# Kernel tuning notes

Hardware: AMD Instinct MI355X
Metric: run time of the kernel (lower is better)

Reference implementation:

```python
import jax, jax.numpy as jnp
import numpy as np

DN = ('NCHW', 'OIHW', 'NCHW')

def conv2d(x, w, b, pad):
    y = jax.lax.conv_general_dilated(x, w, (1, 1), [(pad, pad), (pad, pad)], dimension_numbers=DN)
    return y + b[None, :, None, None]

def setup_inputs() -> dict:
    key = jax.random.key(0)
    ks = jax.random.split(key, 12)
    nc, hc = 10, 16
    B, H, W = 8, 256, 256
    s = 0.1  # small init scale
    return {
        'x': jax.random.normal(ks[0], (B, nc, H, W), dtype=jnp.float32),
        'perceive_w': jax.random.normal(ks[1], (hc * 2, nc + hc, 3, 3), dtype=jnp.float32) * s,
        'perceive_b': jax.random.normal(ks[2], (hc * 2,), dtype=jnp.float32) * s,
        'update1_w': jax.random.normal(ks[3], (hc, hc * 2, 1, 1), dtype=jnp.float32) * s,
        'update1_b': jax.random.normal(ks[4], (hc,), dtype=jnp.float32) * s,
        'update2_w': jax.random.normal(ks[5], (hc, hc, 1, 1), dtype=jnp.float32) * s,
        'update2_b': jax.random.normal(ks[6], (hc,), dtype=jnp.float32) * s,
        'tau_w': jax.random.normal(ks[7], (hc, nc + hc * 2, 3, 3), dtype=jnp.float32) * s,
        'tau_b': jax.random.normal(ks[8], (hc,), dtype=jnp.float32) * s,
        'b_tau': jnp.ones((1, hc, 1, 1), dtype=jnp.float32) * 1.5,
        'readout_w': jax.random.normal(ks[9], (nc, hc, 1, 1), dtype=jnp.float32) * s,
        'readout_b': jax.random.normal(ks[10], (nc,), dtype=jnp.float32) * s,
        'n_steps': 10,
    }

def reference(x, perceive_w, perceive_b, update1_w, update1_b, update2_w, update2_b,
              tau_w, tau_b, b_tau, readout_w, readout_b, n_steps):
    B, _, H, W = x.shape
    hc = update2_w.shape[0]
    state0 = jnp.zeros((B, hc, H, W), dtype=x.dtype)

    def step(state, _):
        combined = jnp.concatenate([x, state], axis=1)          # [B, nc+hc, H, W]
        perception = conv2d(combined, perceive_w, perceive_b, 1)  # [B, 2*hc, H, W]
        hidden = jax.nn.relu(conv2d(perception, update1_w, update1_b, 0))
        delta = conv2d(hidden, update2_w, update2_b, 0)          # [B, hc, H, W]
        tau_input = jnp.concatenate([x, state, delta], axis=1)   # [B, nc+2*hc, H, W]
        beta = jax.nn.sigmoid(conv2d(tau_input, tau_w, tau_b, 1) + b_tau)
        beta = jnp.clip(beta, 0.01, 0.99)
        state = beta * state + (1.0 - beta) * delta
        return state, None

    state, _ = jax.lax.scan(step, state0, None, length=n_steps)
    return conv2d(state, readout_w, readout_b, 0)                # [B, nc, H, W]
```

## Files before the change

### kernel.cpp

```cpp
#include <hip/hip_runtime.h>
#include <math.h>

#define BATCH 8
#define NC 10
#define HC 16
#define HH 256
#define WW 256
#define NSTEPS 10
#define PLANE (HH*WW)

typedef _Float16 v8h  __attribute__((ext_vector_type(8)));
typedef _Float16 v4h  __attribute__((ext_vector_type(4)));
typedef float    v16f __attribute__((ext_vector_type(16)));

#define TW 32
#define TH 8
#define IPW 36
#define IPH 12
#define IPOS (IPW*IPH)
#define ICH 40
#define DPW 34
#define DPH 10
#define DPOS (DPW*DPH)
#define DCH 24

#define MFMA32(A,B,C) __builtin_amdgcn_mfma_f32_32x32x16_f16(A, B, C, 0, 0, 0)

__global__ __launch_bounds__(256) void k_prep(
    const float* __restrict__ x, _Float16* __restrict__ xh)
{
    int g = blockIdx.x * 256 + threadIdx.x;
    int b = g >> 16, pix = g & 65535;
    v8h lo = {0,0,0,0,0,0,0,0}, hi = {0,0,0,0,0,0,0,0};
    #pragma unroll
    for (int c = 0; c < 8; ++c) lo[c] = (_Float16)x[(b*NC + c)*PLANE + pix];
    hi[0] = (_Float16)x[(b*NC + 8)*PLANE + pix];
    hi[1] = (_Float16)x[(b*NC + 9)*PLANE + pix];
    v8h* dst = (v8h*)&xh[(size_t)g * 16];
    dst[0] = lo; dst[1] = hi;
}

__global__ __launch_bounds__(256) void k_repack(
    const float* __restrict__ pw,
    const float* __restrict__ tw,
    const float* __restrict__ u1w, const float* __restrict__ u1b,
    const float* __restrict__ pb,
    const float* __restrict__ u2w,
    _Float16* __restrict__ apD,
    _Float16* __restrict__ apT,
    _Float16* __restrict__ apU1,
    _Float16* __restrict__ apU2,
    float* __restrict__ u1bp)
{
    const int tid = threadIdx.x;
    for (int i = tid; i < 9*2*512; i += 256) {
        int j = i & 7, lane = (i >> 3) & 63, kc = (i >> 9) & 1, t = i >> 10;
        int m = lane & 31, ke = (lane >> 5)*8 + j;
        float v = 0.f;
        if (kc == 1)      v = pw[(m*26 + 10 + ke)*9 + t];
        else if (ke < 10) v = pw[(m*26 + ke)*9 + t];
        apD[i] = (_Float16)v;
    }
    for (int i = tid; i < 9*3*512; i += 256) {
        int j = i & 7, lane = (i >> 3) & 63, r = i >> 9;
        int kc = r % 3, t = r / 3;
        int m = lane & 31, ke = (lane >> 5)*8 + j;
        float v = 0.f;
        if (m < 16) {
            if (kc == 0)      { if (ke < 10) v = tw[(m*42 + ke)*9 + t]; }
            else if (kc == 1) v = tw[(m*42 + 10 + ke)*9 + t];
            else              v = tw[(m*42 + 26 + ke)*9 + t];
        }
        apT[i] = (_Float16)v;
    }
    for (int i = tid; i < 2*2*512; i += 256) {
        int j = i & 7, lane = (i >> 3) & 63, part = (i >> 9) & 1, c = (i >> 10) & 1;
        int m = lane & 31, hh = lane >> 5;
        int ch = 16*c + 4*hh + (j & 3) + 8*(j >> 2);
        float w = (m < 16) ? u1w[m*32 + ch] : 0.f;
        _Float16 hi = (_Float16)w;
        apU1[i] = part ? (_Float16)(w - (float)hi) : hi;
    }
    for (int i = tid; i < 2*512; i += 256) {
        int j = i & 7, lane = (i >> 3) & 63, part = i >> 9;
        int m = lane & 31, hh = lane >> 5;
        int ch = 4*hh + (j & 3) + 8*(j >> 2);
        float w = (m < 16) ? u2w[m*16 + ch] : 0.f;
        _Float16 hi = (_Float16)w;
        apU2[i] = part ? (_Float16)(w - (float)hi) : hi;
    }
    if (tid < 16) {
        float s = u1b[tid];
        for (int p = 0; p < 32; ++p) s += u1w[tid*32 + p] * pb[p];
        u1bp[tid] = s;
    }
}

__device__ __forceinline__ void chain_mfma(
    const v16f A, int p, int h, int by, int bx,
    v8h u1h0, v8h u1r0, v8h u1h1, v8h u1r1,
    v8h u2h, v8h u2r,
    const float* bu1, const float* bu2,
    _Float16* __restrict__ smDl)
{
    v8h b0h, b0r, b1h, b1r;
    #pragma unroll
    for (int j = 0; j < 8; ++j) {
        _Float16 h0 = (_Float16)A[j];
        b0h[j] = h0; b0r[j] = (_Float16)(A[j] - (float)h0);
        _Float16 h1 = (_Float16)A[8 + j];
        b1h[j] = h1; b1r[j] = (_Float16)(A[8 + j] - (float)h1);
    }
    v16f hacc = {0,0,0,0,0,0,0,0,0,0,0,0,0,0,0,0};
    hacc = MFMA32(u1h0, b0h, hacc);
    hacc = MFMA32(u1h0, b0r, hacc);
    hacc = MFMA32(u1r0, b0h, hacc);
    hacc = MFMA32(u1h1, b1h, hacc);
    hacc = MFMA32(u1h1, b1r, hacc);
    hacc = MFMA32(u1r1, b1h, hacc);
    v8h ch_, cr_;
    #pragma unroll
    for (int j = 0; j < 8; ++j) {
        float v = fmaxf(hacc[j] + bu1[j], 0.f);
        _Float16 hh = (_Float16)v;
        ch_[j] = hh; cr_[j] = (_Float16)(v - (float)hh);
    }
    v16f dacc = {0,0,0,0,0,0,0,0,0,0,0,0,0,0,0,0};
    dacc = MFMA32(u2h, ch_, dacc);
    dacc = MFMA32(u2h, cr_, dacc);
    dacc = MFMA32(u2r, ch_, dacc);

    const int yy = p / DPW, xx = p - yy * DPW;
    const int gy = by + yy - 1, gx = bx + xx - 1;
    const bool inImg = (gy >= 0 && gy < HH && gx >= 0 && gx < WW);

    v4h hi0, hi1;
    #pragma unroll
    for (int j = 0; j < 4; ++j) {
        float d0 = inImg ? (dacc[j]     + bu2[j])     : 0.f;
        float d1 = inImg ? (dacc[4 + j] + bu2[4 + j]) : 0.f;
        hi0[j] = (_Float16)d0;
        hi1[j] = (_Float16)d1;
    }
    _Float16* dst = &smDl[p * DCH];
    *(v4h*)(dst + 4*h)     = hi0;
    *(v4h*)(dst + 8 + 4*h) = hi1;
}

__global__ __launch_bounds__(256, 3) void k_step(
    const _Float16* __restrict__ xh,
    const _Float16* __restrict__ shO,
    const _Float16* __restrict__ apD,
    const _Float16* __restrict__ apT,
    const _Float16* __restrict__ apU1,
    const _Float16* __restrict__ apU2,
    const float* __restrict__ u1bp, const float* __restrict__ u2b,
    const float* __restrict__ tb,  const float* __restrict__ btau,
    _Float16* __restrict__ shN,
    const float* __restrict__ rw,  const float* __restrict__ rb,
    float* __restrict__ out, int last)
{
    __shared__ __align__(16) _Float16 smIn[IPOS * ICH];
    __shared__ __align__(16) _Float16 smDl[DPOS * DCH];

    const int tid = threadIdx.x;
    const int bx = blockIdx.x * TW, by = blockIdx.y * TH, b = blockIdx.z;

    for (int i = tid; i < IPOS; i += 256) {
        int yy = i / IPW, xx = i - yy * IPW;
        int gy = by + yy - 2, gx = bx + xx - 2;
        v8h x0 = {0,0,0,0,0,0,0,0}, x1 = x0, s0 = x0, s1 = x0;
        if (gy >= 0 && gy < HH && gx >= 0 && gx < WW) {
            size_t base = ((size_t)((b*HH + gy)*WW + gx)) * 16;
            const v8h* px_ = (const v8h*)&xh[base];
            x0 = px_[0]; x1 = px_[1];
            const v8h* ps_ = (const v8h*)&shO[base];
            s0 = ps_[0]; s1 = ps_[1];
        }
        _Float16* d = &smIn[i * ICH];
        *(v8h*)(d)      = x0;  *(v8h*)(d + 8)  = x1;
        *(v8h*)(d + 16) = s0;  *(v8h*)(d + 24) = s1;
    }

    const int lane = tid & 63, w = tid >> 6;
    const int n = lane & 31, h = lane >> 5;

    v8h u1f00 = *(const v8h*)&apU1[(0*2 + 0)*512 + lane*8];
    v8h u1f01 = *(const v8h*)&apU1[(0*2 + 1)*512 + lane*8];
    v8h u1f10 = *(const v8h*)&apU1[(1*2 + 0)*512 + lane*8];
    v8h u1f11 = *(const v8h*)&apU1[(1*2 + 1)*512 + lane*8];
    v8h u2fh  = *(const v8h*)&apU2[0*512 + lane*8];
    v8h u2fr  = *(const v8h*)&apU2[1*512 + lane*8];
    float bu1[8], bu2[8], btAdd[8];
    #pragma unroll
    for (int j = 0; j < 8; ++j) {
        int m = (j & 3) + 8*(j >> 2) + 4*h;
        bu1[j] = u1bp[m];
        bu2[j] = u2b[m];
        btAdd[j] = tb[m] + btau[m];
    }
    __syncthreads();

    v16f acc0 = {0,0,0,0,0,0,0,0,0,0,0,0,0,0,0,0};
    v16f acc1 = acc0, acc2 = acc0;
    int pA = w*32 + n;           if (pA > DPOS-1) pA = DPOS-1;
    int pB = (w+4)*32 + n;       if (pB > DPOS-1) pB = DPOS-1;
    int pC = (w+8)*32 + n;       if (pC > DPOS-1) pC = DPOS-1;
    const bool hasC = (w < 3);
    int yyA = pA / DPW, xxA = pA - yyA*DPW;
    int yyB = pB / DPW, xxB = pB - yyB*DPW;
    int yyC = pC / DPW, xxC = pC - yyC*DPW;
    int adA = (yyA*IPW + xxA)*(ICH*2) + h*16;
    int adB = (yyB*IPW + xxB)*(ICH*2) + h*16;
    int adC = (yyC*IPW + xxC)*(ICH*2) + h*16;
    const char* smInB = (const char*)smIn;

    #pragma unroll
    for (int t = 0; t < 9; ++t) {
        const int dy = t / 3, dx = t - dy*3;
        const int off = (dy*IPW + dx)*(ICH*2);
        v8h A0 = *(const v8h*)&apD[(t*2 + 0)*512 + lane*8];
        v8h A1 = *(const v8h*)&apD[(t*2 + 1)*512 + lane*8];
        v8h bb;
        bb = *(const v8h*)(smInB + adA + off);      acc0 = MFMA32(A0, bb, acc0);
        bb = *(const v8h*)(smInB + adA + off + 32); acc0 = MFMA32(A1, bb, acc0);
        bb = *(const v8h*)(smInB + adB + off);      acc1 = MFMA32(A0, bb, acc1);
        bb = *(const v8h*)(smInB + adB + off + 32); acc1 = MFMA32(A1, bb, acc1);
        if (hasC) {
            bb = *(const v8h*)(smInB + adC + off);      acc2 = MFMA32(A0, bb, acc2);
            bb = *(const v8h*)(smInB + adC + off + 32); acc2 = MFMA32(A1, bb, acc2);
        }
    }

    chain_mfma(acc0, pA, h, by, bx, u1f00, u1f01, u1f10, u1f11, u2fh, u2fr, bu1, bu2, smDl);
    chain_mfma(acc1, pB, h, by, bx, u1f00, u1f01, u1f10, u1f11, u2fh, u2fr, bu1, bu2, smDl);
    if (hasC)
        chain_mfma(acc2, pC, h, by, bx, u1f00, u1f01, u1f10, u1f11, u2fh, u2fr, bu1, bu2, smDl);
    __syncthreads();

    v16f tc0 = {0,0,0,0,0,0,0,0,0,0,0,0,0,0,0,0};
    v16f tc1 = tc0;
    const int tt0 = w*2, tt1 = w*2 + 1;
    int adI0 = ((tt0 + 1)*IPW + (n + 1))*(ICH*2) + h*16;
    int adI1 = ((tt1 + 1)*IPW + (n + 1))*(ICH*2) + h*16;
    int adD0 = (tt0*DPW + n)*(DCH*2) + h*16;
    int adD1 = (tt1*DPW + n)*(DCH*2) + h*16;
    const char* smDlB = (const char*)smDl;

    #pragma unroll
    for (int t = 0; t < 9; ++t) {
        const int dy = t / 3, dx = t - dy*3;
        const int offI = (dy*IPW + dx)*(ICH*2);
        const int offD = (dy*DPW + dx)*(DCH*2);
        v8h A0 = *(const v8h*)&apT[(t*3 + 0)*512 + lane*8];
        v8h A1 = *(const v8h*)&apT[(t*3 + 1)*512 + lane*8];
        v8h A2 = *(const v8h*)&apT[(t*3 + 2)*512 + lane*8];
        v8h bb;
        bb = *(const v8h*)(smInB + adI0 + offI);      tc0 = MFMA32(A0, bb, tc0);
        bb = *(const v8h*)(smInB + adI0 + offI + 32); tc0 = MFMA32(A1, bb, tc0);
        bb = *(const v8h*)(smDlB + adD0 + offD);      tc0 = MFMA32(A2, bb, tc0);
        bb = *(const v8h*)(smInB + adI1 + offI);      tc1 = MFMA32(A0, bb, tc1);
        bb = *(const v8h*)(smInB + adI1 + offI + 32); tc1 = MFMA32(A1, bb, tc1);
        bb = *(const v8h*)(smDlB + adD1 + offD);      tc1 = MFMA32(A2, bb, tc1);
    }

    #pragma unroll
    for (int g2 = 0; g2 < 2; ++g2) {
        const v16f T = g2 ? tc1 : tc0;
        const int tt = g2 ? tt1 : tt0;
        const int gy = by + tt, gx = bx + n;
        const int dbase = ((tt + 1)*DPW + (n + 1)) * DCH;
        const int ibase = ((tt + 2)*IPW + (n + 2)) * ICH + 16;
        float snv[8];
        #pragma unroll
        for (int mb = 0; mb < 2; ++mb)
            #pragma unroll
            for (int i2 = 0; i2 < 4; ++i2) {
                const int j = mb*4 + i2;
                const int dc = mb*8 + 4*h + i2;
                float v = T[j] + btAdd[j];
                float bt = 1.f / (1.f + __expf(-v));
                bt = fminf(fmaxf(bt, 0.01f), 0.99f);
                float dl = (float)smDl[dbase + dc];
                float so = (float)smIn[ibase + dc];
                snv[j] = bt*so + (1.f - bt)*dl;
            }
        if (!last) {
            size_t pb_ = ((size_t)((b*HH + gy)*WW + gx)) * 16;
            #pragma unroll
            for (int mb = 0; mb < 2; ++mb) {
                v4h q;
                q[0] = (_Float16)snv[mb*4+0]; q[1] = (_Float16)snv[mb*4+1];
                q[2] = (_Float16)snv[mb*4+2]; q[3] = (_Float16)snv[mb*4+3];
                *(v4h*)&shN[pb_ + mb*8 + 4*h] = q;
            }
        } else {
            float rcv[8];
            #pragma unroll
            for (int r = 0; r < 8; ++r) rcv[r] = __shfl_xor(snv[r], 32);
            if (h == 0) {
                #pragma unroll
                for (int o = 0; o < NC; ++o) {
                    float s = rb[o];
                    #pragma unroll
                    for (int mb = 0; mb < 2; ++mb)
                        #pragma unroll
                        for (int i2 = 0; i2 < 4; ++i2) {
                            s = fmaf(snv[mb*4+i2], rw[o*16 + mb*8 + i2],     s);
                            s = fmaf(rcv[mb*4+i2], rw[o*16 + mb*8 + 4 + i2], s);
                        }
                    out[((b*NC + o)*HH + gy)*WW + gx] = s;
                }
            }
        }
    }
}

extern "C" void kernel_launch(void* const* d_in, const int* in_sizes, int n_in,
                              void* d_out, int out_size, void* d_ws, size_t ws_size,
                              hipStream_t stream) {
    const float* x    = (const float*)d_in[0];
    const float* pw   = (const float*)d_in[1];
    const float* pb   = (const float*)d_in[2];
    const float* u1w  = (const float*)d_in[3];
    const float* u1b  = (const float*)d_in[4];
    const float* u2w  = (const float*)d_in[5];
    const float* u2b  = (const float*)d_in[6];
    const float* tw   = (const float*)d_in[7];
    const float* tb   = (const float*)d_in[8];
    const float* btau = (const float*)d_in[9];
    const float* rw   = (const float*)d_in[10];
    const float* rb   = (const float*)d_in[11];

    const size_t planeN = (size_t)BATCH * HC * PLANE;
    _Float16* shA  = (_Float16*)d_ws;
    _Float16* shB  = shA + planeN;
    _Float16* xhp  = shB + planeN;
    _Float16* apD  = xhp + planeN;
    _Float16* apT  = apD + 9*2*512;
    _Float16* apU1 = apT + 9*3*512;
    _Float16* apU2 = apU1 + 2*2*512;
    float*    u1bp = (float*)(apU2 + 2*512);

    hipMemsetAsync(shA, 0, planeN * sizeof(_Float16), stream);

    k_prep<<<BATCH * PLANE / 256, 256, 0, stream>>>(x, xhp);
    k_repack<<<1, 256, 0, stream>>>(pw, tw, u1w, u1b, pb, u2w, apD, apT, apU1, apU2, u1bp);

    dim3 blk(256);
    dim3 grd(WW / TW, HH / TH, BATCH);

    for (int step = 0; step < NSTEPS; ++step) {
        const bool even = (step % 2 == 0);
        const _Float16* shO = even ? shA : shB;
        _Float16*       shN = even ? shB : shA;
        k_step<<<grd, blk, 0, stream>>>(xhp, shO, apD, apT, apU1, apU2,
                                        u1bp, u2b, tb, btau,
                                        shN, rw, rb, (float*)d_out,
                                        step == NSTEPS - 1 ? 1 : 0);
    }
}
```

Before: 499.7 us.

## Precompute step-invariant x contributions of both 3x3 convs once

The input x is constant across all ten steps, so its contribution to the perception conv and to the tau conv is now computed once in a new k_prepC kernel and stored to global memory as fp16. Each step then seeds its accumulators from these buffers and only convolves the state and delta channels. This removes one MFMA chain per tap for the x channels, halves the shared-memory input tile, and raises the occupancy hint. In exchange each step reads extra global buffers, and the stored partial sums are rounded to fp16, which adds some precision error.

```diff
diff --git a/kernel.cpp b/kernel.cpp
--- a/kernel.cpp
+++ b/kernel.cpp
@@ -18,7 +18,7 @@
 #define IPW 36
 #define IPH 12
 #define IPOS (IPW*IPH)
-#define ICH 40
+#define ICH 20
 #define DPW 34
 #define DPH 10
 #define DPOS (DPW*DPH)
@@ -47,31 +47,30 @@
     const float* __restrict__ pb,
     const float* __restrict__ u2w,
     _Float16* __restrict__ apD,
-    _Float16* __restrict__ apT,
+    _Float16* __restrict__ apDx,
+    _Float16* __restrict__ apT2,
+    _Float16* __restrict__ apTx,
     _Float16* __restrict__ apU1,
     _Float16* __restrict__ apU2,
     float* __restrict__ u1bp)
 {
     const int tid = threadIdx.x;
+    for (int i = tid; i < 9*512; i += 256) {
+        int j = i & 7, lane = (i >> 3) & 63, t = i >> 9;
+        int m = lane & 31, ke = (lane >> 5)*8 + j;
+        apD[i]  = (_Float16)pw[(m*26 + 10 + ke)*9 + t];
+        apDx[i] = (_Float16)((ke < 10) ? pw[(m*26 + ke)*9 + t] : 0.f);
+        float vx = 0.f;
+        if (m < 16 && ke < 10) vx = tw[(m*42 + ke)*9 + t];
+        apTx[i] = (_Float16)vx;
+    }
     for (int i = tid; i < 9*2*512; i += 256) {
         int j = i & 7, lane = (i >> 3) & 63, kc = (i >> 9) & 1, t = i >> 10;
         int m = lane & 31, ke = (lane >> 5)*8 + j;
         float v = 0.f;
-        if (kc == 1)      v = pw[(m*26 + 10 + ke)*9 + t];
-        else if (ke < 10) v = pw[(m*26 + ke)*9 + t];
-        apD[i] = (_Float16)v;
-    }
-    for (int i = tid; i < 9*3*512; i += 256) {
-        int j = i & 7, lane = (i >> 3) & 63, r = i >> 9;
-        int kc = r % 3, t = r / 3;
-        int m = lane & 31, ke = (lane >> 5)*8 + j;
-        float v = 0.f;
-        if (m < 16) {
-            if (kc == 0)      { if (ke < 10) v = tw[(m*42 + ke)*9 + t]; }
-            else if (kc == 1) v = tw[(m*42 + 10 + ke)*9 + t];
-            else              v = tw[(m*42 + 26 + ke)*9 + t];
-        }
-        apT[i] = (_Float16)v;
+        if (m < 16) v = kc ? tw[(m*42 + 26 + ke)*9 + t]
+                           : tw[(m*42 + 10 + ke)*9 + t];
+        apT2[i] = (_Float16)v;
     }
     for (int i = tid; i < 2*2*512; i += 256) {
         int j = i & 7, lane = (i >> 3) & 63, part = (i >> 9) & 1, c = (i >> 10) & 1;
@@ -96,72 +95,14 @@
     }
 }
 
-__device__ __forceinline__ void chain_mfma(
-    const v16f A, int p, int h, int by, int bx,
-    v8h u1h0, v8h u1r0, v8h u1h1, v8h u1r1,
-    v8h u2h, v8h u2r,
-    const float* bu1, const float* bu2,
-    _Float16* __restrict__ smDl)
+__global__ __launch_bounds__(256, 4) void k_prepC(
+    const _Float16* __restrict__ xh,
+    const _Float16* __restrict__ apDx,
+    const _Float16* __restrict__ apTx,
+    _Float16* __restrict__ pxc,
+    _Float16* __restrict__ txc)
 {
-    v8h b0h, b0r, b1h, b1r;
-    #pragma unroll
-    for (int j = 0; j < 8; ++j) {
-        _Float16 h0 = (_Float16)A[j];
-        b0h[j] = h0; b0r[j] = (_Float16)(A[j] - (float)h0);
-        _Float16 h1 = (_Float16)A[8 + j];
-        b1h[j] = h1; b1r[j] = (_Float16)(A[8 + j] - (float)h1);
-    }
-    v16f hacc = {0,0,0,0,0,0,0,0,0,0,0,0,0,0,0,0};
-    hacc = MFMA32(u1h0, b0h, hacc);
-    hacc = MFMA32(u1h0, b0r, hacc);
-    hacc = MFMA32(u1r0, b0h, hacc);
-    hacc = MFMA32(u1h1, b1h, hacc);
-    hacc = MFMA32(u1h1, b1r, hacc);
-    hacc = MFMA32(u1r1, b1h, hacc);
-    v8h ch_, cr_;
-    #pragma unroll
-    for (int j = 0; j < 8; ++j) {
-        float v = fmaxf(hacc[j] + bu1[j], 0.f);
-        _Float16 hh = (_Float16)v;
-        ch_[j] = hh; cr_[j] = (_Float16)(v - (float)hh);
-    }
-    v16f dacc = {0,0,0,0,0,0,0,0,0,0,0,0,0,0,0,0};
-    dacc = MFMA32(u2h, ch_, dacc);
-    dacc = MFMA32(u2h, cr_, dacc);
-    dacc = MFMA32(u2r, ch_, dacc);
-
-    const int yy = p / DPW, xx = p - yy * DPW;
-    const int gy = by + yy - 1, gx = bx + xx - 1;
-    const bool inImg = (gy >= 0 && gy < HH && gx >= 0 && gx < WW);
-
-    v4h hi0, hi1;
-    #pragma unroll
-    for (int j = 0; j < 4; ++j) {
-        float d0 = inImg ? (dacc[j]     + bu2[j])     : 0.f;
-        float d1 = inImg ? (dacc[4 + j] + bu2[4 + j]) : 0.f;
-        hi0[j] = (_Float16)d0;
-        hi1[j] = (_Float16)d1;
-    }
-    _Float16* dst = &smDl[p * DCH];
-    *(v4h*)(dst + 4*h)     = hi0;
-    *(v4h*)(dst + 8 + 4*h) = hi1;
-}
-
-__global__ __launch_bounds__(256, 3) void k_step(
-    const _Float16* __restrict__ xh,
-    const _Float16* __restrict__ shO,
-    const _Float16* __restrict__ apD,
-    const _Float16* __restrict__ apT,
-    const _Float16* __restrict__ apU1,
-    const _Float16* __restrict__ apU2,
-    const float* __restrict__ u1bp, const float* __restrict__ u2b,
-    const float* __restrict__ tb,  const float* __restrict__ btau,
-    _Float16* __restrict__ shN,
-    const float* __restrict__ rw,  const float* __restrict__ rb,
-    float* __restrict__ out, int last)
-{
-    __shared__ __align__(16) _Float16 smIn[IPOS * ICH];
-    __shared__ __align__(16) _Float16 smDl[DPOS * DCH];
+    __shared__ __align__(16) _Float16 smX[IPOS * ICH];
 
     const int tid = threadIdx.x;
     const int bx = blockIdx.x * TW, by = blockIdx.y * TH, b = blockIdx.z;
@@ -169,37 +110,19 @@
     for (int i = tid; i < IPOS; i += 256) {
         int yy = i / IPW, xx = i - yy * IPW;
         int gy = by + yy - 2, gx = bx + xx - 2;
-        v8h x0 = {0,0,0,0,0,0,0,0}, x1 = x0, s0 = x0, s1 = x0;
+        v8h x0 = {0,0,0,0,0,0,0,0}, x1 = x0;
         if (gy >= 0 && gy < HH && gx >= 0 && gx < WW) {
             size_t base = ((size_t)((b*HH + gy)*WW + gx)) * 16;
             const v8h* px_ = (const v8h*)&xh[base];
             x0 = px_[0]; x1 = px_[1];
-            const v8h* ps_ = (const v8h*)&shO[base];
-            s0 = ps_[0]; s1 = ps_[1];
-        }
-        _Float16* d = &smIn[i * ICH];
-        *(v8h*)(d)      = x0;  *(v8h*)(d + 8)  = x1;
-        *(v8h*)(d + 16) = s0;  *(v8h*)(d + 24) = s1;
-    }
+        }
+        _Float16* d = &smX[i * ICH];
+        *(v8h*)(d) = x0;  *(v8h*)(d + 8) = x1;
+    }
+    __syncthreads();
 
     const int lane = tid & 63, w = tid >> 6;
     const int n = lane & 31, h = lane >> 5;
-
-    v8h u1f00 = *(const v8h*)&apU1[(0*2 + 0)*512 + lane*8];
-    v8h u1f01 = *(const v8h*)&apU1[(0*2 + 1)*512 + lane*8];
-    v8h u1f10 = *(const v8h*)&apU1[(1*2 + 0)*512 + lane*8];
-    v8h u1f11 = *(const v8h*)&apU1[(1*2 + 1)*512 + lane*8];
-    v8h u2fh  = *(const v8h*)&apU2[0*512 + lane*8];
-    v8h u2fr  = *(const v8h*)&apU2[1*512 + lane*8];
-    float bu1[8], bu2[8], btAdd[8];
-    #pragma unroll
-    for (int j = 0; j < 8; ++j) {
-        int m = (j & 3) + 8*(j >> 2) + 4*h;
-        bu1[j] = u1bp[m];
-        bu2[j] = u2b[m];
-        btAdd[j] = tb[m] + btau[m];
-    }
-    __syncthreads();
 
     v16f acc0 = {0,0,0,0,0,0,0,0,0,0,0,0,0,0,0,0};
     v16f acc1 = acc0, acc2 = acc0;
@@ -213,22 +136,227 @@
     int adA = (yyA*IPW + xxA)*(ICH*2) + h*16;
     int adB = (yyB*IPW + xxB)*(ICH*2) + h*16;
     int adC = (yyC*IPW + xxC)*(ICH*2) + h*16;
-    const char* smInB = (const char*)smIn;
+    const char* smXB = (const char*)smX;
 
     #pragma unroll
     for (int t = 0; t < 9; ++t) {
         const int dy = t / 3, dx = t - dy*3;
         const int off = (dy*IPW + dx)*(ICH*2);
-        v8h A0 = *(const v8h*)&apD[(t*2 + 0)*512 + lane*8];
-        v8h A1 = *(const v8h*)&apD[(t*2 + 1)*512 + lane*8];
+        v8h A0 = *(const v8h*)&apDx[t*512 + lane*8];
         v8h bb;
-        bb = *(const v8h*)(smInB + adA + off);      acc0 = MFMA32(A0, bb, acc0);
-        bb = *(const v8h*)(smInB + adA + off + 32); acc0 = MFMA32(A1, bb, acc0);
-        bb = *(const v8h*)(smInB + adB + off);      acc1 = MFMA32(A0, bb, acc1);
-        bb = *(const v8h*)(smInB + adB + off + 32); acc1 = MFMA32(A1, bb, acc1);
+        bb = *(const v8h*)(smXB + adA + off);  acc0 = MFMA32(A0, bb, acc0);
+        bb = *(const v8h*)(smXB + adB + off);  acc1 = MFMA32(A0, bb, acc1);
         if (hasC) {
-            bb = *(const v8h*)(smInB + adC + off);      acc2 = MFMA32(A0, bb, acc2);
-            bb = *(const v8h*)(smInB + adC + off + 32); acc2 = MFMA32(A1, bb, acc2);
+            bb = *(const v8h*)(smXB + adC + off);  acc2 = MFMA32(A0, bb, acc2);
+        }
+    }
+
+    v16f tc0 = {0,0,0,0,0,0,0,0,0,0,0,0,0,0,0,0};
+    v16f tc1 = tc0;
+    const int tt0 = w*2, tt1 = w*2 + 1;
+    int adI0 = ((tt0 + 1)*IPW + (n + 1))*(ICH*2) + h*16;
+    int adI1 = ((tt1 + 1)*IPW + (n + 1))*(ICH*2) + h*16;
+    #pragma unroll
+    for (int t = 0; t < 9; ++t) {
+        const int dy = t / 3, dx = t - dy*3;
+        const int off = (dy*IPW + dx)*(ICH*2);
+        v8h A0 = *(const v8h*)&apTx[t*512 + lane*8];
+        v8h bb;
+        bb = *(const v8h*)(smXB + adI0 + off);  tc0 = MFMA32(A0, bb, tc0);
+        bb = *(const v8h*)(smXB + adI1 + off);  tc1 = MFMA32(A0, bb, tc1);
+    }
+
+    {
+        const v16f* As[3] = {&acc0, &acc1, &acc2};
+        const int yys[3] = {yyA, yyB, yyC}, xxs[3] = {xxA, xxB, xxC};
+        #pragma unroll
+        for (int q = 0; q < 3; ++q) {
+            if (q == 2 && !hasC) break;
+            const int yy = yys[q], xx = xxs[q];
+            if (yy >= 1 && yy <= 8 && xx >= 1 && xx <= 32) {
+                const int gy = by + yy - 1, gx = bx + xx - 1;
+                const v16f A = *As[q];
+                v8h p0, p1;
+                #pragma unroll
+                for (int j = 0; j < 8; ++j) {
+                    p0[j] = (_Float16)A[j];
+                    p1[j] = (_Float16)A[8 + j];
+                }
+                size_t a = ((size_t)((b*HH + gy)*WW + gx))*32 + 16*h;
+                *(v8h*)&pxc[a]     = p0;
+                *(v8h*)&pxc[a + 8] = p1;
+            }
+        }
+    }
+    #pragma unroll
+    for (int g2 = 0; g2 < 2; ++g2) {
+        const v16f T = g2 ? tc1 : tc0;
+        const int gy = by + (g2 ? tt1 : tt0), gx = bx + n;
+        v4h q0, q1;
+        #pragma unroll
+        for (int j = 0; j < 4; ++j) { q0[j] = (_Float16)T[j]; q1[j] = (_Float16)T[4 + j]; }
+        size_t a = ((size_t)((b*HH + gy)*WW + gx))*16 + 8*h;
+        *(v4h*)&txc[a]     = q0;
+        *(v4h*)&txc[a + 4] = q1;
+    }
+}
+
+__device__ __forceinline__ void chain_mfma(
+    const v16f A, int p, int h, int by, int bx,
+    v8h u1h0, v8h u1r0, v8h u1h1, v8h u1r1,
+    v8h u2h, v8h u2r,
+    const float* bu1, const float* bu2,
+    _Float16* __restrict__ smDl)
+{
+    v8h b0h, b0r, b1h, b1r;
+    #pragma unroll
+    for (int j = 0; j < 8; ++j) {
+        _Float16 h0 = (_Float16)A[j];
+        b0h[j] = h0; b0r[j] = (_Float16)(A[j] - (float)h0);
+        _Float16 h1 = (_Float16)A[8 + j];
+        b1h[j] = h1; b1r[j] = (_Float16)(A[8 + j] - (float)h1);
+    }
+    v16f hacc = {0,0,0,0,0,0,0,0,0,0,0,0,0,0,0,0};
+    hacc = MFMA32(u1h0, b0h, hacc);
+    hacc = MFMA32(u1h0, b0r, hacc);
+    hacc = MFMA32(u1r0, b0h, hacc);
+    hacc = MFMA32(u1h1, b1h, hacc);
+    hacc = MFMA32(u1h1, b1r, hacc);
+    hacc = MFMA32(u1r1, b1h, hacc);
+    v8h ch_, cr_;
+    #pragma unroll
+    for (int j = 0; j < 8; ++j) {
+        float v = fmaxf(hacc[j] + bu1[j], 0.f);
+        _Float16 hh = (_Float16)v;
+        ch_[j] = hh; cr_[j] = (_Float16)(v - (float)hh);
+    }
+    v16f dacc = {0,0,0,0,0,0,0,0,0,0,0,0,0,0,0,0};
+    dacc = MFMA32(u2h, ch_, dacc);
+    dacc = MFMA32(u2h, cr_, dacc);
+    dacc = MFMA32(u2r, ch_, dacc);
+
+    const int yy = p / DPW, xx = p - yy * DPW;
+    const int gy = by + yy - 1, gx = bx + xx - 1;
+    const bool inImg = (gy >= 0 && gy < HH && gx >= 0 && gx < WW);
+
+    v4h hi0, hi1;
+    #pragma unroll
+    for (int j = 0; j < 4; ++j) {
+        float d0 = inImg ? (dacc[j]     + bu2[j])     : 0.f;
+        float d1 = inImg ? (dacc[4 + j] + bu2[4 + j]) : 0.f;
+        hi0[j] = (_Float16)d0;
+        hi1[j] = (_Float16)d1;
+    }
+    _Float16* dst = &smDl[p * DCH];
+    *(v4h*)(dst + 4*h)     = hi0;
+    *(v4h*)(dst + 8 + 4*h) = hi1;
+}
+
+__global__ __launch_bounds__(256, 4) void k_step(
+    const _Float16* __restrict__ shO,
+    const _Float16* __restrict__ apD,
+    const _Float16* __restrict__ apT2,
+    const _Float16* __restrict__ apU1,
+    const _Float16* __restrict__ apU2,
+    const _Float16* __restrict__ pxc,
+    const _Float16* __restrict__ txc,
+    const float* __restrict__ u1bp, const float* __restrict__ u2b,
+    const float* __restrict__ tb,  const float* __restrict__ btau,
+    _Float16* __restrict__ shN,
+    const float* __restrict__ rw,  const float* __restrict__ rb,
+    float* __restrict__ out, int last)
+{
+    __shared__ __align__(16) _Float16 smIn[IPOS * ICH];
+    __shared__ __align__(16) _Float16 smDl[DPOS * DCH];
+
+    const int tid = threadIdx.x;
+    const int bx = blockIdx.x * TW, by = blockIdx.y * TH, b = blockIdx.z;
+
+    for (int i = tid; i < IPOS; i += 256) {
+        int yy = i / IPW, xx = i - yy * IPW;
+        int gy = by + yy - 2, gx = bx + xx - 2;
+        v8h s0 = {0,0,0,0,0,0,0,0}, s1 = s0;
+        if (gy >= 0 && gy < HH && gx >= 0 && gx < WW) {
+            size_t base = ((size_t)((b*HH + gy)*WW + gx)) * 16;
+            const v8h* ps_ = (const v8h*)&shO[base];
+            s0 = ps_[0]; s1 = ps_[1];
+        }
+        _Float16* d = &smIn[i * ICH];
+        *(v8h*)(d) = s0;  *(v8h*)(d + 8) = s1;
+    }
+
+    const int lane = tid & 63, w = tid >> 6;
+    const int n = lane & 31, h = lane >> 5;
+
+    int pA = w*32 + n;           if (pA > DPOS-1) pA = DPOS-1;
+    int pB = (w+4)*32 + n;       if (pB > DPOS-1) pB = DPOS-1;
+    int pC = (w+8)*32 + n;       if (pC > DPOS-1) pC = DPOS-1;
+    const bool hasC = (w < 3);
+    int yyA = pA / DPW, xxA = pA - yyA*DPW;
+    int yyB = pB / DPW, xxB = pB - yyB*DPW;
+    int yyC = pC / DPW, xxC = pC - yyC*DPW;
+    const int tt0 = w*2, tt1 = w*2 + 1;
+
+    v8h pxA0, pxA1, pxB0, pxB1, pxC0 = {0,0,0,0,0,0,0,0}, pxC1 = pxC0;
+    {
+        int cy = min(max(by + yyA - 1, 0), HH-1), cx = min(max(bx + xxA - 1, 0), WW-1);
+        size_t a = ((size_t)((b*HH + cy)*WW + cx))*32 + 16*h;
+        pxA0 = *(const v8h*)&pxc[a]; pxA1 = *(const v8h*)&pxc[a + 8];
+        cy = min(max(by + yyB - 1, 0), HH-1); cx = min(max(bx + xxB - 1, 0), WW-1);
+        a = ((size_t)((b*HH + cy)*WW + cx))*32 + 16*h;
+        pxB0 = *(const v8h*)&pxc[a]; pxB1 = *(const v8h*)&pxc[a + 8];
+        if (hasC) {
+            cy = min(max(by + yyC - 1, 0), HH-1); cx = min(max(bx + xxC - 1, 0), WW-1);
+            a = ((size_t)((b*HH + cy)*WW + cx))*32 + 16*h;
+            pxC0 = *(const v8h*)&pxc[a]; pxC1 = *(const v8h*)&pxc[a + 8];
+        }
+    }
+    v4h tx00, tx01, tx10, tx11;
+    {
+        size_t a0 = ((size_t)((b*HH + by + tt0)*WW + bx + n))*16 + 8*h;
+        tx00 = *(const v4h*)&txc[a0]; tx01 = *(const v4h*)&txc[a0 + 4];
+        size_t a1 = ((size_t)((b*HH + by + tt1)*WW + bx + n))*16 + 8*h;
+        tx10 = *(const v4h*)&txc[a1]; tx11 = *(const v4h*)&txc[a1 + 4];
+    }
+
+    v8h u1f00 = *(const v8h*)&apU1[(0*2 + 0)*512 + lane*8];
+    v8h u1f01 = *(const v8h*)&apU1[(0*2 + 1)*512 + lane*8];
+    v8h u1f10 = *(const v8h*)&apU1[(1*2 + 0)*512 + lane*8];
+    v8h u1f11 = *(const v8h*)&apU1[(1*2 + 1)*512 + lane*8];
+    v8h u2fh  = *(const v8h*)&apU2[0*512 + lane*8];
+    v8h u2fr  = *(const v8h*)&apU2[1*512 + lane*8];
+    float bu1[8], bu2[8], btAdd[8];
+    #pragma unroll
+    for (int j = 0; j < 8; ++j) {
+        int m = (j & 3) + 8*(j >> 2) + 4*h;
+        bu1[j] = u1bp[m];
+        bu2[j] = u2b[m];
+        btAdd[j] = tb[m] + btau[m];
+    }
+    __syncthreads();
+
+    v16f acc0, acc1, acc2;
+    #pragma unroll
+    for (int j = 0; j < 8; ++j) {
+        acc0[j] = (float)pxA0[j]; acc0[8+j] = (float)pxA1[j];
+        acc1[j] = (float)pxB0[j]; acc1[8+j] = (float)pxB1[j];
+        acc2[j] = (float)pxC0[j]; acc2[8+j] = (float)pxC1[j];
+    }
+    int adA = (yyA*IPW + xxA)*(ICH*2) + h*16;
+    int adB = (yyB*IPW + xxB)*(ICH*2) + h*16;
+    int adC = (yyC*IPW + xxC)*(ICH*2) + h*16;
+    const char* smInB = (const char*)smIn;
+
+    #pragma unroll
+    for (int t = 0; t < 9; ++t) {
+        const int dy = t / 3, dx = t - dy*3;
+        const int off = (dy*IPW + dx)*(ICH*2);
+        v8h A0 = *(const v8h*)&apD[t*512 + lane*8];
+        v8h bb;
+        bb = *(const v8h*)(smInB + adA + off);  acc0 = MFMA32(A0, bb, acc0);
+        bb = *(const v8h*)(smInB + adB + off);  acc1 = MFMA32(A0, bb, acc1);
+        if (hasC) {
+            bb = *(const v8h*)(smInB + adC + off);  acc2 = MFMA32(A0, bb, acc2);
         }
     }
 
@@ -240,7 +368,11 @@
 
     v16f tc0 = {0,0,0,0,0,0,0,0,0,0,0,0,0,0,0,0};
     v16f tc1 = tc0;
-    const int tt0 = w*2, tt1 = w*2 + 1;
+    #pragma unroll
+    for (int j = 0; j < 4; ++j) {
+        tc0[j] = (float)tx00[j]; tc0[4+j] = (float)tx01[j];
+        tc1[j] = (float)tx10[j]; tc1[4+j] = (float)tx11[j];
+    }
     int adI0 = ((tt0 + 1)*IPW + (n + 1))*(ICH*2) + h*16;
     int adI1 = ((tt1 + 1)*IPW + (n + 1))*(ICH*2) + h*16;
     int adD0 = (tt0*DPW + n)*(DCH*2) + h*16;
@@ -252,16 +384,13 @@
         const int dy = t / 3, dx = t - dy*3;
         const int offI = (dy*IPW + dx)*(ICH*2);
         const int offD = (dy*DPW + dx)*(DCH*2);
-        v8h A0 = *(const v8h*)&apT[(t*3 + 0)*512 + lane*8];
-        v8h A1 = *(const v8h*)&apT[(t*3 + 1)*512 + lane*8];
-        v8h A2 = *(const v8h*)&apT[(t*3 + 2)*512 + lane*8];
+        v8h A0 = *(const v8h*)&apT2[(t*2 + 0)*512 + lane*8];
+        v8h A1 = *(const v8h*)&apT2[(t*2 + 1)*512 + lane*8];
         v8h bb;
-        bb = *(const v8h*)(smInB + adI0 + offI);      tc0 = MFMA32(A0, bb, tc0);
-        bb = *(const v8h*)(smInB + adI0 + offI + 32); tc0 = MFMA32(A1, bb, tc0);
-        bb = *(const v8h*)(smDlB + adD0 + offD);      tc0 = MFMA32(A2, bb, tc0);
-        bb = *(const v8h*)(smInB + adI1 + offI);      tc1 = MFMA32(A0, bb, tc1);
-        bb = *(const v8h*)(smInB + adI1 + offI + 32); tc1 = MFMA32(A1, bb, tc1);
-        bb = *(const v8h*)(smDlB + adD1 + offD);      tc1 = MFMA32(A2, bb, tc1);
+        bb = *(const v8h*)(smInB + adI0 + offI);  tc0 = MFMA32(A0, bb, tc0);
+        bb = *(const v8h*)(smDlB + adD0 + offD);  tc0 = MFMA32(A1, bb, tc0);
+        bb = *(const v8h*)(smInB + adI1 + offI);  tc1 = MFMA32(A0, bb, tc1);
+        bb = *(const v8h*)(smDlB + adD1 + offD);  tc1 = MFMA32(A1, bb, tc1);
     }
 
     #pragma unroll
@@ -270,7 +399,7 @@
         const int tt = g2 ? tt1 : tt0;
         const int gy = by + tt, gx = bx + n;
         const int dbase = ((tt + 1)*DPW + (n + 1)) * DCH;
-        const int ibase = ((tt + 2)*IPW + (n + 2)) * ICH + 16;
+        const int ibase = ((tt + 2)*IPW + (n + 2)) * ICH;
         float snv[8];
         #pragma unroll
         for (int mb = 0; mb < 2; ++mb)
@@ -336,25 +465,32 @@
     _Float16* shA  = (_Float16*)d_ws;
     _Float16* shB  = shA + planeN;
     _Float16* xhp  = shB + planeN;
-    _Float16* apD  = xhp + planeN;
-    _Float16* apT  = apD + 9*2*512;
-    _Float16* apU1 = apT + 9*3*512;
+    _Float16* pxc  = xhp + planeN;
+    _Float16* txc  = pxc + 2*planeN;
+    _Float16* apD  = txc + planeN;
+    _Float16* apDx = apD + 9*512;
+    _Float16* apT2 = apDx + 9*512;
+    _Float16* apTx = apT2 + 18*512;
+    _Float16* apU1 = apTx + 9*512;
     _Float16* apU2 = apU1 + 2*2*512;
     float*    u1bp = (float*)(apU2 + 2*512);
 
     hipMemsetAsync(shA, 0, planeN * sizeof(_Float16), stream);
 
     k_prep<<<BATCH * PLANE / 256, 256, 0, stream>>>(x, xhp);
-    k_repack<<<1, 256, 0, stream>>>(pw, tw, u1w, u1b, pb, u2w, apD, apT, apU1, apU2, u1bp);
+    k_repack<<<1, 256, 0, stream>>>(pw, tw, u1w, u1b, pb, u2w,
+                                    apD, apDx, apT2, apTx, apU1, apU2, u1bp);
 
     dim3 blk(256);
     dim3 grd(WW / TW, HH / TH, BATCH);
+
+    k_prepC<<<grd, blk, 0, stream>>>(xhp, apDx, apTx, pxc, txc);
 
     for (int step = 0; step < NSTEPS; ++step) {
         const bool even = (step % 2 == 0);
         const _Float16* shO = even ? shA : shB;
         _Float16*       shN = even ? shB : shA;
-        k_step<<<grd, blk, 0, stream>>>(xhp, shO, apD, apT, apU1, apU2,
+        k_step<<<grd, blk, 0, stream>>>(shO, apD, apT2, apU1, apU2, pxc, txc,
                                         u1bp, u2b, tb, btau,
                                         shN, rw, rb, (float*)d_out,
                                         step == NSTEPS - 1 ? 1 : 0);
```

Result: slower. 763.1 us (+52.7%).
